# Kernel optimization log

Hardware: AMD Instinct MI355X
Metric: run time of the kernel (lower is better)

Reference implementation:

```python
import jax, jax.numpy as jnp
import numpy as np

BATCH, T, N = 8, 2048, 512


def setup_inputs() -> dict:
    key = jax.random.key(0)
    ks = jax.random.split(key, 8)
    scale = 1.0 / np.sqrt(2.0 * (N + N) / 2.0) / np.sqrt(2.0)  # GlorotNormal / sqrt(2)
    u = jax.random.normal(ks[0], (BATCH, T, N), dtype=jnp.float32)
    C_re = jax.random.normal(ks[1], (N, N), dtype=jnp.float32) * scale
    C_im = jax.random.normal(ks[2], (N, N), dtype=jnp.float32) * scale
    B_re = jax.random.normal(ks[3], (N, N), dtype=jnp.float32) * scale
    B_im = jax.random.normal(ks[4], (N, N), dtype=jnp.float32) * scale
    D = jax.random.normal(ks[5], (N,), dtype=jnp.float32)
    # nu drawn from the numerically-stable end of [log(-log rmax), log(-log rmin)]
    nu = jax.random.uniform(ks[6], (N,), minval=-4.6, maxval=-3.7, dtype=jnp.float32)
    theta = jax.random.uniform(ks[7], (N,), minval=0.0, maxval=3.14 / 10, dtype=jnp.float32)
    # gamma initialized as sqrt(1 - |lambda|^2), lambda = exp(-exp(nu) + i*theta)
    gamma = jnp.sqrt(1.0 - jnp.exp(-2.0 * jnp.exp(nu)))
    return {"u": u, "C_re": C_re, "C_im": C_im, "B_re": B_re, "B_im": B_im,
            "D": D, "nu": nu, "theta": theta, "gamma": gamma}


def reference(u, C_re, C_im, B_re, B_im, D, nu, theta, gamma):
    # log_lambda = -exp(nu) + i*theta  (the TF code names this `lambda_`)
    log_lam = (-jnp.exp(nu)).astype(jnp.complex64) + 1j * theta.astype(jnp.complex64)  # (n,)
    t = jnp.arange(u.shape[1], dtype=jnp.float32).astype(jnp.complex64)[:, None]       # (T,1)
    lam_pow = jnp.exp(log_lam[None, :] * t)    # (T,n) == diag(Lambda^t)
    lam_minpow = jnp.exp(-log_lam[None, :] * t)  # (T,n) == diag(Lambda^-t)
    Bm = (B_re + 1j * B_im).astype(jnp.complex64)  # (n,n)
    Cm = (C_re + 1j * C_im).astype(jnp.complex64)  # (n,n)
    # new_u = (gamma * u) @ B   (complex)
    new_u = (gamma * u).astype(jnp.complex64) @ Bm  # (b,t,n)
    # diag einsums in the original are elementwise multiplies
    x = jnp.cumsum(new_u * lam_minpow[None], axis=1) * lam_pow[None]  # (b,t,n)
    y = jnp.real(x @ Cm) + D * u
    return y
```

## Files before the change

kernel.cpp:

```cpp
#include <hip/hip_runtime.h>
#include <hip/hip_bf16.h>
#include <math.h>
#include <stdint.h>

#define BATCH 8
#define T_LEN 2048
#define NDIM 512
#define M_ROWS (BATCH * T_LEN)
#define CHUNK 32
#define NCHUNK (T_LEN / CHUNK)

typedef __attribute__((ext_vector_type(8))) short bf16x8;
typedef __attribute__((ext_vector_type(4))) float floatx4;

__device__ __forceinline__ unsigned short f2bf(float f) {
    union { float f; unsigned u; } v; v.f = f;
    unsigned r = v.u + 0x7fff + ((v.u >> 16) & 1);
    return (unsigned short)(r >> 16);
}
__device__ __forceinline__ float bf2f(unsigned short h) {
    union { unsigned u; float f; } v; v.u = ((unsigned)h) << 16;
    return v.f;
}
__device__ __forceinline__ float bf2f_lo(unsigned u) {
    union { unsigned u; float f; } v; v.u = u << 16; return v.f;
}
__device__ __forceinline__ float bf2f_hi(unsigned u) {
    union { unsigned u; float f; } v; v.u = u & 0xffff0000u; return v.f;
}

__device__ __forceinline__ void gld_lds16(const unsigned short* g, unsigned short* l) {
    __builtin_amdgcn_global_load_lds(
        (const __attribute__((address_space(1))) unsigned int*)(uintptr_t)g,
        (__attribute__((address_space(3))) unsigned int*)(uintptr_t)l,
        16, 0, 0);
}

__global__ __launch_bounds__(256) void k_prep(
    const float* __restrict__ u,
    const float* __restrict__ Bre, const float* __restrict__ Bim,
    const float* __restrict__ Cre, const float* __restrict__ Cim,
    const float* __restrict__ gamma,
    unsigned short* __restrict__ ubf,
    unsigned short* __restrict__ BT, unsigned short* __restrict__ CT)
{
    __shared__ unsigned short tile[32][33];
    const int blk = blockIdx.x;
    if (blk < 4096) {
        size_t i = ((size_t)blk * 256 + threadIdx.x) * 8;
        float4 a = *(const float4*)&u[i];
        float4 b = *(const float4*)&u[i + 4];
        ushort4 p0, p1;
        p0.x = f2bf(a.x); p0.y = f2bf(a.y); p0.z = f2bf(a.z); p0.w = f2bf(a.w);
        p1.x = f2bf(b.x); p1.y = f2bf(b.y); p1.z = f2bf(b.z); p1.w = f2bf(b.w);
        *(ushort4*)&ubf[i] = p0;
        *(ushort4*)&ubf[i + 4] = p1;
        return;
    }
    const int p = blk - 4096;
    const int z = p >> 8;
    const int rem = p & 255;
    const int n0 = (rem & 15) * 32, k0 = (rem >> 4) * 32;
    const float* __restrict__ src = (z == 0) ? Bre : (z == 1) ? Bim : (z == 2) ? Cre : Cim;
    const int tx = threadIdx.x & 31, ty = threadIdx.x >> 5;

#pragma unroll
    for (int j = 0; j < 4; ++j) {
        int k = k0 + ty + j * 8;
        float s = (z < 2) ? gamma[k] : (z == 3 ? -1.f : 1.f);
        tile[ty + j * 8][tx] = f2bf(s * src[(size_t)k * NDIM + n0 + tx]);
    }
    __syncthreads();
#pragma unroll
    for (int j = 0; j < 4; ++j) {
        int n = n0 + ty + j * 8;
        unsigned short v = tile[tx][ty + j * 8];
        if (z == 0)      BT[(size_t)n * 512 + k0 + tx] = v;
        else if (z == 1) BT[(size_t)(512 + n) * 512 + k0 + tx] = v;
        else if (z == 2) CT[(size_t)n * 1024 + k0 + tx] = v;
        else             CT[(size_t)n * 1024 + 512 + k0 + tx] = v;
    }
}

__global__ __launch_bounds__(256) void k_gemm_in(
    const unsigned short* __restrict__ A,
    const unsigned short* __restrict__ BT,
    unsigned short* __restrict__ X)
{
    __shared__ unsigned short As[128 * 32];
    __shared__ unsigned short Bs[128 * 32];
    const int tid = threadIdx.x;
    const int w = tid >> 6, l = tid & 63;
    const int bm = blockIdx.x * 128;
    const int bn = blockIdx.y * 128;
    const int wm = (w & 1) * 64, wn = (w >> 1) * 64;
    const int lm = l & 15, lq = l >> 4;
    const int srow = w * 16 + (l >> 2);
    const int scol = (l & 3) * 8;

    floatx4 acc[4][4];
#pragma unroll
    for (int i = 0; i < 4; ++i)
#pragma unroll
        for (int j = 0; j < 4; ++j) acc[i][j] = (floatx4)0.f;

    for (int k0 = 0; k0 < 512; k0 += 32) {
        gld_lds16(&A[(size_t)(bm + srow) * 512 + k0 + scol],      &As[srow * 32 + scol]);
        gld_lds16(&A[(size_t)(bm + 64 + srow) * 512 + k0 + scol], &As[(64 + srow) * 32 + scol]);
        gld_lds16(&BT[(size_t)(bn + srow) * 512 + k0 + scol],      &Bs[srow * 32 + scol]);
        gld_lds16(&BT[(size_t)(bn + 64 + srow) * 512 + k0 + scol], &Bs[(64 + srow) * 32 + scol]);
        __syncthreads();

        bf16x8 af[4], bfr[4];
#pragma unroll
        for (int i = 0; i < 4; ++i)
            af[i] = *(const bf16x8*)&As[(wm + i * 16 + lm) * 32 + lq * 8];
#pragma unroll
        for (int j = 0; j < 4; ++j)
            bfr[j] = *(const bf16x8*)&Bs[(wn + j * 16 + lm) * 32 + lq * 8];
#pragma unroll
        for (int i = 0; i < 4; ++i)
#pragma unroll
            for (int j = 0; j < 4; ++j)
                acc[i][j] = __builtin_amdgcn_mfma_f32_16x16x32_bf16(af[i], bfr[j], acc[i][j], 0, 0, 0);
        __syncthreads();
    }

#pragma unroll
    for (int i = 0; i < 4; ++i)
#pragma unroll
        for (int j = 0; j < 4; ++j) {
            int col = bn + wn + j * 16 + lm;
#pragma unroll
            for (int r = 0; r < 4; ++r) {
                int row = bm + wm + i * 16 + lq * 4 + r;
                X[(size_t)row * 1024 + col] = f2bf(acc[i][j][r]);
            }
        }
}

__global__ __launch_bounds__(256) void k_scan_carries(
    const unsigned short* __restrict__ X,
    const float* __restrict__ nu, const float* __restrict__ theta,
    float* __restrict__ carry)
{
    const int n0 = 2 * threadIdx.x;
    const int b = blockIdx.x >> 6, c = blockIdx.x & 63;
    float r0 = __expf(-__expf(nu[n0]));
    float r1 = __expf(-__expf(nu[n0 + 1]));
    float lre0 = r0 * __cosf(theta[n0]),     lim0 = r0 * __sinf(theta[n0]);
    float lre1 = r1 * __cosf(theta[n0 + 1]), lim1 = r1 * __sinf(theta[n0 + 1]);
    size_t m = (size_t)b * T_LEN + (size_t)c * CHUNK;
    float xre0 = 0.f, xim0 = 0.f, xre1 = 0.f, xim1 = 0.f;
#pragma unroll 8
    for (int t = 0; t < CHUNK; ++t, ++m) {
        unsigned re = *(const unsigned*)&X[m * 1024 + n0];
        unsigned im = *(const unsigned*)&X[m * 1024 + 512 + n0];
        float u0 = bf2f_lo(re), u1 = bf2f_hi(re);
        float v0 = bf2f_lo(im), v1 = bf2f_hi(im);
        float a0 = lre0 * xre0 - lim0 * xim0 + u0;
        float b0 = lre0 * xim0 + lim0 * xre0 + v0;
        float a1 = lre1 * xre1 - lim1 * xim1 + u1;
        float b1 = lre1 * xim1 + lim1 * xre1 + v1;
        xre0 = a0; xim0 = b0; xre1 = a1; xim1 = b1;
    }
    size_t ci = ((size_t)b * NCHUNK + c) * NDIM + n0;
    *(float4*)&carry[ci * 2] = make_float4(xre0, xim0, xre1, xim1);
}

__global__ __launch_bounds__(256) void k_scan_chain(
    const float* __restrict__ carry,
    const float* __restrict__ nu, const float* __restrict__ theta,
    float* __restrict__ pre)
{
    const int tid = blockIdx.x * blockDim.x + threadIdx.x;
    const int b = tid >> 9, n = tid & (NDIM - 1);
    const float ex = __expf(nu[n]);
    const float rC = expf(-ex * (float)CHUNK);
    const float th = theta[n] * (float)CHUNK;
    const float a = rC * cosf(th);
    const float bb = rC * sinf(th);
    float Xre = 0.f, Xim = 0.f;
    for (int c = 0; c < NCHUNK; ++c) {
        size_t idx = ((size_t)b * NCHUNK + c) * NDIM + n;
        *(float2*)&pre[idx * 2] = make_float2(Xre, Xim);
        float2 cv = *(const float2*)&carry[idx * 2];
        float nre = a * Xre - bb * Xim + cv.x;
        float nim = a * Xim + bb * Xre + cv.y;
        Xre = nre; Xim = nim;
    }
}

__global__ __launch_bounds__(256) void k_scan_apply(
    unsigned short* __restrict__ X,
    const float* __restrict__ nu, const float* __restrict__ theta,
    const float* __restrict__ pre)
{
    const int n0 = 2 * threadIdx.x;
    const int b = blockIdx.x >> 6, c = blockIdx.x & 63;
    size_t pi = ((size_t)b * NCHUNK + c) * NDIM + n0;
    float4 P = *(const float4*)&pre[pi * 2];
    float r0 = __expf(-__expf(nu[n0]));
    float r1 = __expf(-__expf(nu[n0 + 1]));
    float lre0 = r0 * __cosf(theta[n0]),     lim0 = r0 * __sinf(theta[n0]);
    float lre1 = r1 * __cosf(theta[n0 + 1]), lim1 = r1 * __sinf(theta[n0 + 1]);
    float xre0 = P.x, xim0 = P.y, xre1 = P.z, xim1 = P.w;
    size_t m = (size_t)b * T_LEN + (size_t)c * CHUNK;
#pragma unroll 8
    for (int t = 0; t < CHUNK; ++t, ++m) {
        unsigned re = *(const unsigned*)&X[m * 1024 + n0];
        unsigned im = *(const unsigned*)&X[m * 1024 + 512 + n0];
        float u0 = bf2f_lo(re), u1 = bf2f_hi(re);
        float v0 = bf2f_lo(im), v1 = bf2f_hi(im);
        float a0 = lre0 * xre0 - lim0 * xim0 + u0;
        float b0 = lre0 * xim0 + lim0 * xre0 + v0;
        float a1 = lre1 * xre1 - lim1 * xim1 + u1;
        float b1 = lre1 * xim1 + lim1 * xre1 + v1;
        xre0 = a0; xim0 = b0; xre1 = a1; xim1 = b1;
        unsigned pr = (unsigned)f2bf(xre0) | ((unsigned)f2bf(xre1) << 16);
        unsigned pim = (unsigned)f2bf(xim0) | ((unsigned)f2bf(xim1) << 16);
        *(unsigned*)&X[m * 1024 + n0] = pr;
        *(unsigned*)&X[m * 1024 + 512 + n0] = pim;
    }
}

__global__ __launch_bounds__(256) void k_gemm_out(
    const unsigned short* __restrict__ Xbf,
    const unsigned short* __restrict__ CT,
    const float* __restrict__ D,
    const unsigned short* __restrict__ Ubf,
    float* __restrict__ Y)
{
    __shared__ unsigned short As[64 * 32];
    __shared__ unsigned short Bs[128 * 32];
    const int tid = threadIdx.x;
    const int w = tid >> 6, l = tid & 63;
    const int bm = blockIdx.x * 64;
    const int bn = blockIdx.y * 128;
    const int wm = (w & 1) * 32, wn = (w >> 1) * 64;
    const int lm = l & 15, lq = l >> 4;
    const int arow = tid >> 2;
    const int acol = (tid & 3) * 8;
    const int srow = w * 16 + (l >> 2);
    const int scol = (l & 3) * 8;

    floatx4 acc[2][4];
#pragma unroll
    for (int i = 0; i < 2; ++i)
#pragma unroll
        for (int j = 0; j < 4; ++j) acc[i][j] = (floatx4)0.f;

    for (int k0 = 0; k0 < 1024; k0 += 32) {
        gld_lds16(&Xbf[(size_t)(bm + arow) * 1024 + k0 + acol],     &As[arow * 32 + acol]);
        gld_lds16(&CT[(size_t)(bn + srow) * 1024 + k0 + scol],      &Bs[srow * 32 + scol]);
        gld_lds16(&CT[(size_t)(bn + 64 + srow) * 1024 + k0 + scol], &Bs[(64 + srow) * 32 + scol]);
        __syncthreads();

        bf16x8 af[2], bfr[4];
#pragma unroll
        for (int i = 0; i < 2; ++i)
            af[i] = *(const bf16x8*)&As[(wm + i * 16 + lm) * 32 + lq * 8];
#pragma unroll
        for (int j = 0; j < 4; ++j)
            bfr[j] = *(const bf16x8*)&Bs[(wn + j * 16 + lm) * 32 + lq * 8];
#pragma unroll
        for (int i = 0; i < 2; ++i)
#pragma unroll
            for (int j = 0; j < 4; ++j)
                acc[i][j] = __builtin_amdgcn_mfma_f32_16x16x32_bf16(af[i], bfr[j], acc[i][j], 0, 0, 0);
        __syncthreads();
    }

#pragma unroll
    for (int i = 0; i < 2; ++i)
#pragma unroll
        for (int j = 0; j < 4; ++j) {
            int col = bn + wn + j * 16 + lm;
            float dv = D[col];
#pragma unroll
            for (int r = 0; r < 4; ++r) {
                int row = bm + wm + i * 16 + lq * 4 + r;
                size_t off = (size_t)row * NDIM + col;
                Y[off] = acc[i][j][r] + dv * bf2f(Ubf[off]);
            }
        }
}

extern "C" void kernel_launch(void* const* d_in, const int* in_sizes, int n_in,
                              void* d_out, int out_size, void* d_ws, size_t ws_size,
                              hipStream_t stream)
{
    const float* u     = (const float*)d_in[0];
    const float* C_re  = (const float*)d_in[1];
    const float* C_im  = (const float*)d_in[2];
    const float* B_re  = (const float*)d_in[3];
    const float* B_im  = (const float*)d_in[4];
    const float* D     = (const float*)d_in[5];
    const float* nu    = (const float*)d_in[6];
    const float* theta = (const float*)d_in[7];
    const float* gamma = (const float*)d_in[8];
    float* y = (float*)d_out;

    unsigned short* X   = (unsigned short*)d_ws;
    unsigned short* ubf = X + (size_t)M_ROWS * 1024;
    unsigned short* BT  = ubf + (size_t)M_ROWS * 512;
    unsigned short* CT  = BT + (size_t)1024 * 512;
    float* carry = (float*)(CT + (size_t)512 * 1024);
    float* pre   = carry + (size_t)BATCH * NCHUNK * NDIM * 2;

    k_prep<<<4096 + 1024, 256, 0, stream>>>(u, B_re, B_im, C_re, C_im, gamma, ubf, BT, CT);
    k_gemm_in<<<dim3(M_ROWS / 128, 8), 256, 0, stream>>>(ubf, BT, X);
    k_scan_carries<<<BATCH * NCHUNK, 256, 0, stream>>>(X, nu, theta, carry);
    k_scan_chain<<<(BATCH * NDIM) / 256, 256, 0, stream>>>(carry, nu, theta, pre);
    k_scan_apply<<<BATCH * NCHUNK, 256, 0, stream>>>(X, nu, theta, pre);
    k_gemm_out<<<dim3(M_ROWS / 64, 4), 256, 0, stream>>>(X, CT, D, ubf, y);
}
```

Baseline: 179.1 us.

## Fuse intra-chunk scan into input GEMM epilogue with interleaved complex layout

Interleaves real and imaginary columns of B and C so each GEMM tile holds complete complex pairs, then runs the within-chunk recurrence on the tile in LDS inside the input GEMM epilogue and writes locally scanned X plus chunk carries. The apply pass becomes a non-recurrent correction that adds lambda^t times the chunk prefix, skips chunk zero and uses vector loads. The output GEMM stages its accumulators through LDS so that Y, D and u are accessed with coalesced vector loads and stores. This removes a full read of X and the separate carry kernel, at the cost of extra LDS use and synchronisation in the GEMM epilogues.

Result: no change. 177.8 us (-0.7%).

```diff
diff --git a/kernel.cpp b/kernel.cpp
--- a/kernel.cpp
+++ b/kernel.cpp
@@ -9,6 +9,7 @@
 #define M_ROWS (BATCH * T_LEN)
 #define CHUNK 32
 #define NCHUNK (T_LEN / CHUNK)
+
 
 typedef __attribute__((ext_vector_type(8))) short bf16x8;
 typedef __attribute__((ext_vector_type(4))) float floatx4;
@@ -75,20 +76,24 @@
     for (int j = 0; j < 4; ++j) {
         int n = n0 + ty + j * 8;
         unsigned short v = tile[tx][ty + j * 8];
-        if (z == 0)      BT[(size_t)n * 512 + k0 + tx] = v;
-        else if (z == 1) BT[(size_t)(512 + n) * 512 + k0 + tx] = v;
-        else if (z == 2) CT[(size_t)n * 1024 + k0 + tx] = v;
-        else             CT[(size_t)n * 1024 + 512 + k0 + tx] = v;
-    }
-}
-
-__global__ __launch_bounds__(256) void k_gemm_in(
+        if (z < 2)   BT[(size_t)(2 * n + z) * 512 + k0 + tx] = v;
+        else         CT[(size_t)n * 1024 + 2 * (k0 + tx) + (z - 2)] = v;
+    }
+}
+
+#define XS_STRIDE 136
+__global__ __launch_bounds__(256) void k_gemm_in_scan(
     const unsigned short* __restrict__ A,
     const unsigned short* __restrict__ BT,
-    unsigned short* __restrict__ X)
-{
-    __shared__ unsigned short As[128 * 32];
-    __shared__ unsigned short Bs[128 * 32];
+    const float* __restrict__ nu, const float* __restrict__ theta,
+    unsigned short* __restrict__ X,
+    float* __restrict__ carry)
+{
+    __shared__ __align__(16) unsigned short smem[128 * XS_STRIDE];
+    unsigned short* As = smem;
+    unsigned short* Bs = smem + 4096;
+    unsigned short* Xs = smem;
+
     const int tid = threadIdx.x;
     const int w = tid >> 6, l = tid & 63;
     const int bm = blockIdx.x * 128;
@@ -130,42 +135,47 @@
     for (int i = 0; i < 4; ++i)
 #pragma unroll
         for (int j = 0; j < 4; ++j) {
-            int col = bn + wn + j * 16 + lm;
+            int col = wn + j * 16 + lm;
 #pragma unroll
             for (int r = 0; r < 4; ++r) {
-                int row = bm + wm + i * 16 + lq * 4 + r;
-                X[(size_t)row * 1024 + col] = f2bf(acc[i][j][r]);
+                int row = wm + i * 16 + lq * 4 + r;
+                Xs[row * XS_STRIDE + col] = f2bf(acc[i][j][r]);
             }
         }
-}
-
-__global__ __launch_bounds__(256) void k_scan_carries(
-    const unsigned short* __restrict__ X,
-    const float* __restrict__ nu, const float* __restrict__ theta,
-    float* __restrict__ carry)
-{
-    const int n0 = 2 * threadIdx.x;
-    const int b = blockIdx.x >> 6, c = blockIdx.x & 63;
-    float r0 = __expf(-__expf(nu[n0]));
-    float r1 = __expf(-__expf(nu[n0 + 1]));
-    float lre0 = r0 * __cosf(theta[n0]),     lim0 = r0 * __sinf(theta[n0]);
-    float lre1 = r1 * __cosf(theta[n0 + 1]), lim1 = r1 * __sinf(theta[n0 + 1]);
-    size_t m = (size_t)b * T_LEN + (size_t)c * CHUNK;
-    float xre0 = 0.f, xim0 = 0.f, xre1 = 0.f, xim1 = 0.f;
+    __syncthreads();
+
+    {
+        const int cc = tid >> 6;
+        const int ch = tid & 63;
+        const int n  = (bn >> 1) + ch;
+        const int b  = bm >> 11;
+        const int c  = ((bm & 2047) >> 5) + cc;
+        const float rr  = __expf(-__expf(nu[n]));
+        const float lre = rr * __cosf(theta[n]);
+        const float lim = rr * __sinf(theta[n]);
+        float xre = 0.f, xim = 0.f;
+        int base = (cc * 32) * XS_STRIDE + 2 * ch;
 #pragma unroll 8
-    for (int t = 0; t < CHUNK; ++t, ++m) {
-        unsigned re = *(const unsigned*)&X[m * 1024 + n0];
-        unsigned im = *(const unsigned*)&X[m * 1024 + 512 + n0];
-        float u0 = bf2f_lo(re), u1 = bf2f_hi(re);
-        float v0 = bf2f_lo(im), v1 = bf2f_hi(im);
-        float a0 = lre0 * xre0 - lim0 * xim0 + u0;
-        float b0 = lre0 * xim0 + lim0 * xre0 + v0;
-        float a1 = lre1 * xre1 - lim1 * xim1 + u1;
-        float b1 = lre1 * xim1 + lim1 * xre1 + v1;
-        xre0 = a0; xim0 = b0; xre1 = a1; xim1 = b1;
-    }
-    size_t ci = ((size_t)b * NCHUNK + c) * NDIM + n0;
-    *(float4*)&carry[ci * 2] = make_float4(xre0, xim0, xre1, xim1);
+        for (int t = 0; t < 32; ++t) {
+            unsigned v = *(const unsigned*)&Xs[base + t * XS_STRIDE];
+            float nre = lre * xre - lim * xim + bf2f_lo(v);
+            float nim = lre * xim + lim * xre + bf2f_hi(v);
+            xre = nre; xim = nim;
+            *(unsigned*)&Xs[base + t * XS_STRIDE] =
+                (unsigned)f2bf(xre) | ((unsigned)f2bf(xim) << 16);
+        }
+        size_t ci = ((size_t)b * NCHUNK + c) * NDIM + n;
+        *(float2*)&carry[ci * 2] = make_float2(xre, xim);
+    }
+    __syncthreads();
+
+#pragma unroll
+    for (int it = 0; it < 8; ++it) {
+        int row = (tid >> 4) + 16 * it;
+        int cs  = (tid & 15) * 8;
+        uint4 v = *(const uint4*)&Xs[row * XS_STRIDE + cs];
+        *(uint4*)&X[(size_t)(bm + row) * 1024 + bn + cs] = v;
+    }
 }
 
 __global__ __launch_bounds__(256) void k_scan_chain(
@@ -196,34 +206,36 @@
     const float* __restrict__ nu, const float* __restrict__ theta,
     const float* __restrict__ pre)
 {
-    const int n0 = 2 * threadIdx.x;
     const int b = blockIdx.x >> 6, c = blockIdx.x & 63;
+    if (c == 0) return;
+    const int t2 = threadIdx.x;
+    const int n0 = 2 * t2;
     size_t pi = ((size_t)b * NCHUNK + c) * NDIM + n0;
     float4 P = *(const float4*)&pre[pi * 2];
     float r0 = __expf(-__expf(nu[n0]));
     float r1 = __expf(-__expf(nu[n0 + 1]));
     float lre0 = r0 * __cosf(theta[n0]),     lim0 = r0 * __sinf(theta[n0]);
     float lre1 = r1 * __cosf(theta[n0 + 1]), lim1 = r1 * __sinf(theta[n0 + 1]);
-    float xre0 = P.x, xim0 = P.y, xre1 = P.z, xim1 = P.w;
+    float fre0 = lre0, fim0 = lim0, fre1 = lre1, fim1 = lim1;
     size_t m = (size_t)b * T_LEN + (size_t)c * CHUNK;
 #pragma unroll 8
     for (int t = 0; t < CHUNK; ++t, ++m) {
-        unsigned re = *(const unsigned*)&X[m * 1024 + n0];
-        unsigned im = *(const unsigned*)&X[m * 1024 + 512 + n0];
-        float u0 = bf2f_lo(re), u1 = bf2f_hi(re);
-        float v0 = bf2f_lo(im), v1 = bf2f_hi(im);
-        float a0 = lre0 * xre0 - lim0 * xim0 + u0;
-        float b0 = lre0 * xim0 + lim0 * xre0 + v0;
-        float a1 = lre1 * xre1 - lim1 * xim1 + u1;
-        float b1 = lre1 * xim1 + lim1 * xre1 + v1;
-        xre0 = a0; xim0 = b0; xre1 = a1; xim1 = b1;
-        unsigned pr = (unsigned)f2bf(xre0) | ((unsigned)f2bf(xre1) << 16);
-        unsigned pim = (unsigned)f2bf(xim0) | ((unsigned)f2bf(xim1) << 16);
-        *(unsigned*)&X[m * 1024 + n0] = pr;
-        *(unsigned*)&X[m * 1024 + 512 + n0] = pim;
-    }
-}
-
+        uint2 v = *(const uint2*)&X[m * 1024 + n0 * 2];
+        float xre0 = bf2f_lo(v.x) + (fre0 * P.x - fim0 * P.y);
+        float xim0 = bf2f_hi(v.x) + (fre0 * P.y + fim0 * P.x);
+        float xre1 = bf2f_lo(v.y) + (fre1 * P.z - fim1 * P.w);
+        float xim1 = bf2f_hi(v.y) + (fre1 * P.w + fim1 * P.z);
+        uint2 o;
+        o.x = (unsigned)f2bf(xre0) | ((unsigned)f2bf(xim0) << 16);
+        o.y = (unsigned)f2bf(xre1) | ((unsigned)f2bf(xim1) << 16);
+        *(uint2*)&X[m * 1024 + n0 * 2] = o;
+        float a0 = fre0 * lre0 - fim0 * lim0, b0 = fre0 * lim0 + fim0 * lre0;
+        float a1 = fre1 * lre1 - fim1 * lim1, b1 = fre1 * lim1 + fim1 * lre1;
+        fre0 = a0; fim0 = b0; fre1 = a1; fim1 = b1;
+    }
+}
+
+#define YS_STRIDE 132
 __global__ __launch_bounds__(256) void k_gemm_out(
     const unsigned short* __restrict__ Xbf,
     const unsigned short* __restrict__ CT,
@@ -231,8 +243,11 @@
     const unsigned short* __restrict__ Ubf,
     float* __restrict__ Y)
 {
-    __shared__ unsigned short As[64 * 32];
-    __shared__ unsigned short Bs[128 * 32];
+    __shared__ __align__(16) char smem[64 * YS_STRIDE * 4];
+    unsigned short* As = (unsigned short*)smem;
+    unsigned short* Bs = (unsigned short*)(smem + 4096);
+    float* Ys = (float*)smem;
+
     const int tid = threadIdx.x;
     const int w = tid >> 6, l = tid & 63;
     const int bm = blockIdx.x * 64;
@@ -275,15 +290,29 @@
     for (int i = 0; i < 2; ++i)
 #pragma unroll
         for (int j = 0; j < 4; ++j) {
-            int col = bn + wn + j * 16 + lm;
-            float dv = D[col];
+            int col = wn + j * 16 + lm;
 #pragma unroll
             for (int r = 0; r < 4; ++r) {
-                int row = bm + wm + i * 16 + lq * 4 + r;
-                size_t off = (size_t)row * NDIM + col;
-                Y[off] = acc[i][j][r] + dv * bf2f(Ubf[off]);
+                int row = wm + i * 16 + lq * 4 + r;
+                Ys[row * YS_STRIDE + col] = acc[i][j][r];
             }
         }
+    __syncthreads();
+
+#pragma unroll
+    for (int it = 0; it < 8; ++it) {
+        int row = (tid >> 5) + 8 * it;
+        int cs  = (tid & 31) * 4;
+        float4 a = *(const float4*)&Ys[row * YS_STRIDE + cs];
+        float4 d = *(const float4*)&D[bn + cs];
+        uint2 uv = *(const uint2*)&Ubf[(size_t)(bm + row) * 512 + bn + cs];
+        float4 o;
+        o.x = a.x + d.x * bf2f_lo(uv.x);
+        o.y = a.y + d.y * bf2f_hi(uv.x);
+        o.z = a.z + d.z * bf2f_lo(uv.y);
+        o.w = a.w + d.w * bf2f_hi(uv.y);
+        *(float4*)&Y[(size_t)(bm + row) * 512 + bn + cs] = o;
+    }
 }
 
 extern "C" void kernel_launch(void* const* d_in, const int* in_sizes, int n_in,
@@ -309,8 +338,7 @@
     float* pre   = carry + (size_t)BATCH * NCHUNK * NDIM * 2;
 
     k_prep<<<4096 + 1024, 256, 0, stream>>>(u, B_re, B_im, C_re, C_im, gamma, ubf, BT, CT);
-    k_gemm_in<<<dim3(M_ROWS / 128, 8), 256, 0, stream>>>(ubf, BT, X);
-    k_scan_carries<<<BATCH * NCHUNK, 256, 0, stream>>>(X, nu, theta, carry);
+    k_gemm_in_scan<<<dim3(M_ROWS / 128, 8), 256, 0, stream>>>(ubf, BT, nu, theta, X, carry);
     k_scan_chain<<<(BATCH * NDIM) / 256, 256, 0, stream>>>(carry, nu, theta, pre);
     k_scan_apply<<<BATCH * NCHUNK, 256, 0, stream>>>(X, nu, theta, pre);
     k_gemm_out<<<dim3(M_ROWS / 64, 4), 256, 0, stream>>>(X, CT, D, ubf, y);
```
